# Kernel tuning notes

Hardware: AMD Instinct MI355X
Metric: run time of the kernel (lower is better)

The kernel has to match this reference:

```python
import jax, jax.numpy as jnp
import numpy as np

D_MODEL = 512
N_HEADS = 8
HEAD_DIM = D_MODEL // N_HEADS
B, T = 2, 4096


def setup_inputs() -> dict:
    key = jax.random.key(0)
    k1, k2, k3 = jax.random.split(key, 3)
    scale = 1.0 / np.sqrt(D_MODEL)
    return {
        "x": jax.random.normal(k1, (B, T, D_MODEL), dtype=jnp.float32),
        "w_qkv": jax.random.normal(k2, (D_MODEL, 3 * D_MODEL), dtype=jnp.float32) * scale,
        "b_qkv": jnp.zeros((3 * D_MODEL,), dtype=jnp.float32),
        "w_out": jax.random.normal(k3, (D_MODEL, D_MODEL), dtype=jnp.float32) * scale,
        "b_out": jnp.zeros((D_MODEL,), dtype=jnp.float32),
    }


def reference(x, w_qkv, b_qkv, w_out, b_out):
    Bx, Tx, C = x.shape
    # fused qkv projection -> [B, T, 3, H, Dh] -> split
    qkv = (x @ w_qkv + b_qkv).reshape(Bx, Tx, 3, N_HEADS, HEAD_DIM)
    q = qkv[:, :, 0].transpose(0, 2, 1, 3)  # [B, H, T, Dh]
    k = qkv[:, :, 1].transpose(0, 2, 1, 3)
    v = qkv[:, :, 2].transpose(0, 2, 1, 3)
    # scaled scores with causal mask (materialized [B,H,T,T], as in source)
    att = jnp.einsum("bhqd,bhkd->bhqk", q, k) * (HEAD_DIM ** -0.5)
    causal = jnp.tril(jnp.ones((Tx, Tx), dtype=bool))
    att = jnp.where(causal[None, None], att, -jnp.inf)
    att = jax.nn.softmax(att, axis=-1)
    # dropout = 0.0 (inference-deterministic baseline)
    y = jnp.einsum("bhqk,bhkd->bhqd", att, v)  # [B, H, T, Dh]
    y = y.transpose(0, 2, 1, 3).reshape(Bx, Tx, C)
    return y @ w_out + b_out
```

## Files before the change

### kernel.cpp

```cpp
#include <hip/hip_runtime.h>
#include <cstdint>
#include <cstddef>

typedef __attribute__((ext_vector_type(8)))  __bf16 bf16x8;
typedef __attribute__((ext_vector_type(4)))  float  f32x4;
typedef __attribute__((ext_vector_type(16))) float  f32x16;

#define MFMA16(a, b, c) __builtin_amdgcn_mfma_f32_16x16x32_bf16((a), (b), (c), 0, 0, 0)
#define MFMA32(a, b, c) __builtin_amdgcn_mfma_f32_32x32x16_bf16((a), (b), (c), 0, 0, 0)

#define T_SEQ 4096
#define NHEADS 8
#define DH 64
#define NROWS (2 * NHEADS * T_SEQ)
#define NSPLIT 4
#define NEG_INF (-__builtin_huge_valf())
#define SCALE_Q 0.18033688011112042f

__device__ __forceinline__ unsigned short f2bf(float f) {
  unsigned int u = __float_as_uint(f);
  u += 0x7fffu + ((u >> 16) & 1u);
  return (unsigned short)(u >> 16);
}

__device__ __forceinline__ unsigned int cvtpk(float lo, float hi) {
  unsigned int r;
  asm("v_cvt_pk_bf16_f32 %0, %1, %2" : "=v"(r) : "v"(lo), "v"(hi));
  return r;
}

__device__ __forceinline__ void swap32(unsigned int& x, unsigned int& y) {
  asm("v_permlane32_swap_b32 %0, %1" : "+v"(x), "+v"(y));
}

__device__ __forceinline__ unsigned int pack_bf2(float a, float b) {
  unsigned int au = __float_as_uint(a) + 0x8000u;
  unsigned int bu = __float_as_uint(b) + 0x8000u;
  return (au >> 16) | (bu & 0xffff0000u);
}

__device__ __forceinline__ void gload16(const unsigned short* g, unsigned short* l) {
  __builtin_amdgcn_global_load_lds(
      (const __attribute__((address_space(1))) unsigned short*)g,
      (__attribute__((address_space(3))) unsigned short*)l, 16, 0, 0);
}

__global__ void cvt_x_kernel(const float* __restrict__ x,
                             unsigned short* __restrict__ xb, int n4) {
  int i = blockIdx.x * blockDim.x + threadIdx.x;
  if (i >= n4) return;
  float4 v = ((const float4*)x)[i];
  ushort4 o;
  o.x = f2bf(v.x); o.y = f2bf(v.y); o.z = f2bf(v.z); o.w = f2bf(v.w);
  ((ushort4*)xb)[i] = o;
}

__global__ void cvt_T_kernel(const float* __restrict__ w,
                             unsigned short* __restrict__ wT, int N, int total) {
  int i = blockIdx.x * blockDim.x + threadIdx.x;
  if (i >= total) return;
  int n = i >> 9, k = i & 511;
  wT[i] = f2bf(w[(size_t)k * N + n]);
}

template <int EPI>
__global__ __launch_bounds__(256) void gemm_bt(
    const unsigned short* __restrict__ A,
    const unsigned short* __restrict__ BT,
    const float* __restrict__ bias,
    float* __restrict__ outf,
    unsigned short* __restrict__ oq,
    unsigned short* __restrict__ ok,
    unsigned short* __restrict__ ovT,
    int K) {
  __shared__ alignas(16) unsigned short As[128 * 32];
  __shared__ alignas(16) unsigned short Bs[128 * 32];

  const int t = threadIdx.x;
  const int lane = t & 63;
  const int w = t >> 6;
  const int wr = (w >> 1) * 64;
  const int wc = (w & 1) * 64;
  const int g = lane >> 4, c = lane & 15;
  const int row0 = blockIdx.y * 128, col0 = blockIdx.x * 128;

  const int crow = t >> 2;
  const int ccol = (t & 3) * 8;
  const unsigned short* Ag0 = A + (size_t)(row0 + crow) * K + ccol;
  const unsigned short* Ag1 = A + (size_t)(row0 + 64 + crow) * K + ccol;
  const unsigned short* Bg0 = BT + (size_t)(col0 + crow) * K + ccol;
  const unsigned short* Bg1 = BT + (size_t)(col0 + 64 + crow) * K + ccol;

  f32x4 acc[4][4] = {};

  for (int k0 = 0; k0 < K; k0 += 32) {
    int4 a0 = *(const int4*)(Ag0 + k0);
    int4 a1 = *(const int4*)(Ag1 + k0);
    int4 b0 = *(const int4*)(Bg0 + k0);
    int4 b1 = *(const int4*)(Bg1 + k0);
    __syncthreads();
    *(int4*)&As[crow * 32 + ccol] = a0;
    *(int4*)&As[(64 + crow) * 32 + ccol] = a1;
    *(int4*)&Bs[crow * 32 + ccol] = b0;
    *(int4*)&Bs[(64 + crow) * 32 + ccol] = b1;
    __syncthreads();

    bf16x8 af[4], bfr[4];
#pragma unroll
    for (int m = 0; m < 4; ++m)
      af[m] = *(const bf16x8*)&As[(wr + m * 16 + c) * 32 + g * 8];
#pragma unroll
    for (int n = 0; n < 4; ++n)
      bfr[n] = *(const bf16x8*)&Bs[(wc + n * 16 + c) * 32 + g * 8];
#pragma unroll
    for (int m = 0; m < 4; ++m)
#pragma unroll
      for (int n = 0; n < 4; ++n)
        acc[m][n] = MFMA16(af[m], bfr[n], acc[m][n]);
  }

#pragma unroll
  for (int m = 0; m < 4; ++m) {
#pragma unroll
    for (int n = 0; n < 4; ++n) {
      const int col = col0 + wc + n * 16 + c;
      const float bv = bias[col];
      if constexpr (EPI == 0) {
        const int which = col >> 9;
        const int h = (col >> 6) & 7;
        const int dh = col & 63;
        const int r0 = row0 + wr + m * 16 + g * 4;
        const int bb = r0 >> 12;
        const int tt0 = r0 & 4095;
        if (which == 2) {
          ushort4 pk;
          pk.x = f2bf(acc[m][n][0] + bv);
          pk.y = f2bf(acc[m][n][1] + bv);
          pk.z = f2bf(acc[m][n][2] + bv);
          pk.w = f2bf(acc[m][n][3] + bv);
          *(ushort4*)&ovT[((size_t)((bb * NHEADS + h) * DH + dh)) * T_SEQ + tt0] = pk;
        } else {
          unsigned short* dst = (which == 0) ? oq : ok;
          const float sc = (which == 0) ? SCALE_Q : 1.0f;
#pragma unroll
          for (int i = 0; i < 4; ++i) {
            const size_t idx =
                ((size_t)((bb * NHEADS + h) * T_SEQ + tt0 + i)) * DH + dh;
            dst[idx] = f2bf((acc[m][n][i] + bv) * sc);
          }
        }
      } else {
#pragma unroll
        for (int i = 0; i < 4; ++i) {
          const int row = row0 + wr + m * 16 + g * 4 + i;
          outf[(size_t)row * 512 + col] = acc[m][n][i] + bv;
        }
      }
    }
  }
}

__global__ __launch_bounds__(256, 4) void attn_kernel(
    const unsigned short* __restrict__ qb,
    const unsigned short* __restrict__ kb,
    const unsigned short* __restrict__ vtb,
    unsigned short* __restrict__ opart,
    float* __restrict__ sb) {
  const int bh = blockIdx.x;
  const int y = blockIdx.y;
  const int hv = blockIdx.z;
  const int w = threadIdx.x >> 6;
  const int lane = threadIdx.x & 63;
  const int q32 = lane & 31;
  const int h = lane >> 5;
  const int swb = (lane & 7) << 4;

  __shared__ alignas(16) unsigned short Ks[2][64 * 64];
  __shared__ alignas(16) unsigned short Vs[2][64 * 64];

  const unsigned short* Qp  = qb + (size_t)bh * T_SEQ * DH;
  const unsigned short* Kp  = kb + (size_t)bh * T_SEQ * DH;
  const unsigned short* VTp = vtb + (size_t)bh * DH * T_SEQ;

  unsigned short* obh = opart + (size_t)hv * NROWS * DH;
  float* sbh = sb + (size_t)hv * NROWS + (size_t)bh * T_SEQ;

  const int l8 = lane >> 3, lc = lane & 7;
  const int swzE = 8 * (lc ^ l8);
  const unsigned short* Ksrc0 = Kp + (size_t)(16 * w + l8) * DH + swzE;
  const unsigned short* Ksrc1 = Kp + (size_t)(16 * w + 8 + l8) * DH + swzE;
  const unsigned short* Vsrc0 = VTp + (size_t)(16 * w + l8) * T_SEQ + swzE;
  const unsigned short* Vsrc1 = VTp + (size_t)(16 * w + 8 + l8) * T_SEQ + swzE;

#define STAGE(B, J0) do {                                              \
    gload16(Ksrc0 + (size_t)(J0) * DH, &Ks[B][(2 * w) * 512]);         \
    gload16(Ksrc1 + (size_t)(J0) * DH, &Ks[B][(2 * w + 1) * 512]);     \
    gload16(Vsrc0 + (J0), &Vs[B][(2 * w) * 512]);                      \
    gload16(Vsrc1 + (J0), &Vs[B][(2 * w + 1) * 512]);                  \
  } while (0)

  for (int pass = 0; pass < 2; ++pass) {
    const int sbk = pass ? (31 - y) : y;
    const int qw = sbk * 128 + w * 32;
    const int ntp = 2 * sbk + 2;
    const int t0 = (ntp * hv) >> 2;
    const int t1 = (ntp * (hv + 1)) >> 2;
    const int tlast = (qw + 31) >> 6;

    bf16x8 qf[4];
#pragma unroll
    for (int d = 0; d < 4; ++d)
      qf[d] = *(const bf16x8*)&Qp[(size_t)(qw + q32) * DH + 16 * d + 8 * h];

    f32x16 acc0 = {}, acc1 = {};
    float mi = NEG_INF;
    float li = 0.f;

    STAGE(0, t0 * 64);
    __syncthreads();
    int cur = 0;

    for (int t = t0; t < t1; ++t) {
      if (t + 1 < t1) STAGE(cur ^ 1, (t + 1) * 64);

      if (t <= tlast) {
        const char* Kb = (const char*)&Ks[cur][0];
        const char* Vb = (const char*)&Vs[cur][0];

        f32x16 s0 = {}, s1 = {};
#pragma unroll
        for (int d = 0; d < 4; ++d) {
          bf16x8 kf0 = *(const bf16x8*)(Kb + q32 * 128 +
                                        ((32 * d + 16 * h) ^ swb));
          bf16x8 kf1 = *(const bf16x8*)(Kb + (32 + q32) * 128 +
                                        ((32 * d + 16 * h) ^ swb));
          s0 = MFMA32(kf0, qf[d], s0);
          s1 = MFMA32(kf1, qf[d], s1);
        }

        if (t == tlast) {
          const int qq = qw + q32;
          const int kb0 = t * 64 + 4 * h;
#pragma unroll
          for (int r = 0; r < 16; ++r) {
            const int ko = kb0 + (r & 3) + 8 * (r >> 2);
            if (ko > qq) s0[r] = NEG_INF;
            if (ko + 32 > qq) s1[r] = NEG_INF;
          }
        }

        float mv[8];
#pragma unroll
        for (int i = 0; i < 8; ++i)
          mv[i] = fmaxf(fmaxf(s0[2 * i], s0[2 * i + 1]),
                        fmaxf(s1[2 * i], s1[2 * i + 1]));
        float mloc = fmaxf(fmaxf(fmaxf(mv[0], mv[1]), fmaxf(mv[2], mv[3])),
                           fmaxf(fmaxf(mv[4], mv[5]), fmaxf(mv[6], mv[7])));
        mloc = fmaxf(mloc, __shfl_xor(mloc, 32));

        if (__ballot(mloc > mi + 8.0f) != 0ull) {
          const float mn = fmaxf(mi, mloc);
          const float scq = exp2f(mi - mn);
          mi = mn;
          li *= scq;
#pragma unroll
          for (int r = 0; r < 16; ++r) { acc0[r] *= scq; acc1[r] *= scq; }
        }

        float ls = 0.f;
#pragma unroll
        for (int kk = 0; kk < 4; ++kk) {
          float pv[8];
#pragma unroll
          for (int e = 0; e < 8; ++e) {
            const float sv = (kk < 2) ? s0[(kk & 1) * 8 + e]
                                      : s1[(kk & 1) * 8 + e];
            pv[e] = exp2f(sv - mi);
          }
          ls += ((pv[0] + pv[1]) + (pv[2] + pv[3])) +
                ((pv[4] + pv[5]) + (pv[6] + pv[7]));
          unsigned int a0 = cvtpk(pv[0], pv[1]);
          unsigned int a1 = cvtpk(pv[2], pv[3]);
          unsigned int b0 = cvtpk(pv[4], pv[5]);
          unsigned int b1 = cvtpk(pv[6], pv[7]);
          swap32(a0, b0);
          swap32(a1, b1);
          union { unsigned int u[4]; bf16x8 v; } pf;
          pf.u[0] = a0; pf.u[1] = a1; pf.u[2] = b0; pf.u[3] = b1;

          bf16x8 vf0 = *(const bf16x8*)(Vb + q32 * 128 +
                                        ((32 * kk + 16 * h) ^ swb));
          bf16x8 vf1 = *(const bf16x8*)(Vb + (32 + q32) * 128 +
                                        ((32 * kk + 16 * h) ^ swb));
          acc0 = MFMA32(vf0, pf.v, acc0);
          acc1 = MFMA32(vf1, pf.v, acc1);
        }
        ls += __shfl_xor(ls, 32);
        li += ls;
      }

      __syncthreads();
      cur ^= 1;
    }

    if (lane < 32) sbh[qw + lane] = (li > 0.f) ? (mi + log2f(li)) : NEG_INF;
    const float inv = (li > 0.f) ? 1.0f / li : 0.f;
    const size_t base = ((size_t)bh * T_SEQ + qw + q32) * DH;
#pragma unroll
    for (int dt = 0; dt < 2; ++dt) {
#pragma unroll
      for (int p4 = 0; p4 < 4; ++p4) {
        const float v0 = (dt ? acc1[4 * p4 + 0] : acc0[4 * p4 + 0]) * inv;
        const float v1 = (dt ? acc1[4 * p4 + 1] : acc0[4 * p4 + 1]) * inv;
        const float v2 = (dt ? acc1[4 * p4 + 2] : acc0[4 * p4 + 2]) * inv;
        const float v3 = (dt ? acc1[4 * p4 + 3] : acc0[4 * p4 + 3]) * inv;
        const int d0 = 32 * dt + 8 * p4 + 4 * h;
        *(unsigned int*)&obh[base + d0]     = cvtpk(v0, v1);
        *(unsigned int*)&obh[base + d0 + 2] = cvtpk(v2, v3);
      }
    }
  }
#undef STAGE
}

__global__ __launch_bounds__(256) void merge_kernel(
    const unsigned short* __restrict__ opart,
    const float* __restrict__ sb,
    unsigned short* __restrict__ yb) {
  const int t = threadIdx.x;
  const int r = blockIdx.x * 32 + (t >> 3);
  const int dseg = (t & 7) * 8;
  float s[NSPLIT];
#pragma unroll
  for (int i = 0; i < NSPLIT; ++i) s[i] = sb[(size_t)i * NROWS + r];
  const float S = fmaxf(fmaxf(s[0], s[1]), fmaxf(s[2], s[3]));
  float a[NSPLIT], wsum = 0.f;
#pragma unroll
  for (int i = 0; i < NSPLIT; ++i) { a[i] = exp2f(s[i] - S); wsum += a[i]; }
  const float inv = 1.0f / wsum;
  float acc[8] = {};
#pragma unroll
  for (int i = 0; i < NSPLIT; ++i) {
    const float ai = a[i] * inv;
    const uint4 u = *(const uint4*)&opart[(size_t)i * NROWS * DH +
                                          (size_t)r * DH + dseg];
    const unsigned int* pu = (const unsigned int*)&u;
#pragma unroll
    for (int j = 0; j < 4; ++j) {
      acc[2 * j]     += ai * __uint_as_float(pu[j] << 16);
      acc[2 * j + 1] += ai * __uint_as_float(pu[j] & 0xffff0000u);
    }
  }
  unsigned int ow[4];
#pragma unroll
  for (int j = 0; j < 4; ++j) ow[j] = pack_bf2(acc[2 * j], acc[2 * j + 1]);
  const int bh = r >> 12, q = r & 4095;
  const int bb = bh >> 3, hh = bh & 7;
  *(uint4*)&yb[((size_t)(bb * T_SEQ + q)) * 512 + hh * DH + dseg] = *(uint4*)ow;
}

extern "C" void kernel_launch(void* const* d_in, const int* in_sizes, int n_in,
                              void* d_out, int out_size, void* d_ws, size_t ws_size,
                              hipStream_t stream) {
  const float* x     = (const float*)d_in[0];
  const float* w_qkv = (const float*)d_in[1];
  const float* b_qkv = (const float*)d_in[2];
  const float* w_out = (const float*)d_in[3];
  const float* b_out = (const float*)d_in[4];
  float* out = (float*)d_out;

  char* p = (char*)d_ws;
  unsigned short* xb    = (unsigned short*)p; p += (size_t)8192 * 512 * 2;
  unsigned short* wqkvT = (unsigned short*)p; p += (size_t)1536 * 512 * 2;
  unsigned short* woutT = (unsigned short*)p; p += (size_t)512 * 512 * 2;
  unsigned short* qbuf  = (unsigned short*)p; p += (size_t)16 * T_SEQ * DH * 2;
  unsigned short* kbuf  = (unsigned short*)p; p += (size_t)16 * T_SEQ * DH * 2;
  unsigned short* vtbuf = (unsigned short*)p; p += (size_t)16 * T_SEQ * DH * 2;
  unsigned short* ybuf  = (unsigned short*)p; p += (size_t)8192 * 512 * 2;
  unsigned short* opart = (unsigned short*)p; p += (size_t)NSPLIT * NROWS * DH * 2;
  float*          sbuf  = (float*)p;          p += (size_t)NSPLIT * NROWS * 4;

  cvt_x_kernel<<<4096, 256, 0, stream>>>(x, xb, 8192 * 512 / 4);
  cvt_T_kernel<<<3072, 256, 0, stream>>>(w_qkv, wqkvT, 1536, 1536 * 512);
  cvt_T_kernel<<<1024, 256, 0, stream>>>(w_out, woutT, 512, 512 * 512);

  gemm_bt<0><<<dim3(12, 64), 256, 0, stream>>>(xb, wqkvT, b_qkv, nullptr,
                                               qbuf, kbuf, vtbuf, 512);
  attn_kernel<<<dim3(16, 16, NSPLIT), 256, 0, stream>>>(qbuf, kbuf, vtbuf,
                                                        opart, sbuf);
  merge_kernel<<<NROWS / 32, 256, 0, stream>>>(opart, sbuf, ybuf);
  gemm_bt<1><<<dim3(4, 64), 256, 0, stream>>>(ybuf, woutT, b_out, out,
                                              nullptr, nullptr, nullptr, 512);
}
```

Measured before the change: 138.1 us.

## Double-buffer GEMM LDS tiles with direct global-to-LDS prefetch

```diff
diff --git a/kernel.cpp b/kernel.cpp
--- a/kernel.cpp
+++ b/kernel.cpp
@@ -73,8 +73,8 @@
     unsigned short* __restrict__ ok,
     unsigned short* __restrict__ ovT,
     int K) {
-  __shared__ alignas(16) unsigned short As[128 * 32];
-  __shared__ alignas(16) unsigned short Bs[128 * 32];
+  __shared__ alignas(16) unsigned short As[2][128 * 32];
+  __shared__ alignas(16) unsigned short Bs[2][128 * 32];
 
   const int t = threadIdx.x;
   const int lane = t & 63;
@@ -84,40 +84,46 @@
   const int g = lane >> 4, c = lane & 15;
   const int row0 = blockIdx.y * 128, col0 = blockIdx.x * 128;
 
-  const int crow = t >> 2;
-  const int ccol = (t & 3) * 8;
-  const unsigned short* Ag0 = A + (size_t)(row0 + crow) * K + ccol;
-  const unsigned short* Ag1 = A + (size_t)(row0 + 64 + crow) * K + ccol;
-  const unsigned short* Bg0 = BT + (size_t)(col0 + crow) * K + ccol;
-  const unsigned short* Bg1 = BT + (size_t)(col0 + 64 + crow) * K + ccol;
+  const int sr = t >> 2;
+  const int sc = (t & 3) * 8;
+  const unsigned short* Asrc0 = A + (size_t)(row0 + sr) * K + sc;
+  const unsigned short* Asrc1 = A + (size_t)(row0 + 64 + sr) * K + sc;
+  const unsigned short* Bsrc0 = BT + (size_t)(col0 + sr) * K + sc;
+  const unsigned short* Bsrc1 = BT + (size_t)(col0 + 64 + sr) * K + sc;
+
+#define STAGE_G(B, K0) do {                                    \
+    gload16(Asrc0 + (K0), &As[B][w * 512]);                    \
+    gload16(Asrc1 + (K0), &As[B][2048 + w * 512]);             \
+    gload16(Bsrc0 + (K0), &Bs[B][w * 512]);                    \
+    gload16(Bsrc1 + (K0), &Bs[B][2048 + w * 512]);             \
+  } while (0)
 
   f32x4 acc[4][4] = {};
 
+  STAGE_G(0, 0);
+  __syncthreads();
+  int cur = 0;
+
   for (int k0 = 0; k0 < K; k0 += 32) {
-    int4 a0 = *(const int4*)(Ag0 + k0);
-    int4 a1 = *(const int4*)(Ag1 + k0);
-    int4 b0 = *(const int4*)(Bg0 + k0);
-    int4 b1 = *(const int4*)(Bg1 + k0);
-    __syncthreads();
-    *(int4*)&As[crow * 32 + ccol] = a0;
-    *(int4*)&As[(64 + crow) * 32 + ccol] = a1;
-    *(int4*)&Bs[crow * 32 + ccol] = b0;
-    *(int4*)&Bs[(64 + crow) * 32 + ccol] = b1;
-    __syncthreads();
+    if (k0 + 32 < K) STAGE_G(cur ^ 1, k0 + 32);
 
     bf16x8 af[4], bfr[4];
 #pragma unroll
     for (int m = 0; m < 4; ++m)
-      af[m] = *(const bf16x8*)&As[(wr + m * 16 + c) * 32 + g * 8];
+      af[m] = *(const bf16x8*)&As[cur][(wr + m * 16 + c) * 32 + g * 8];
 #pragma unroll
     for (int n = 0; n < 4; ++n)
-      bfr[n] = *(const bf16x8*)&Bs[(wc + n * 16 + c) * 32 + g * 8];
+      bfr[n] = *(const bf16x8*)&Bs[cur][(wc + n * 16 + c) * 32 + g * 8];
 #pragma unroll
     for (int m = 0; m < 4; ++m)
 #pragma unroll
       for (int n = 0; n < 4; ++n)
         acc[m][n] = MFMA16(af[m], bfr[n], acc[m][n]);
+
+    __syncthreads();
+    cur ^= 1;
   }
+#undef STAGE_G
 
 #pragma unroll
   for (int m = 0; m < 4; ++m) {
@@ -141,12 +147,12 @@
           *(ushort4*)&ovT[((size_t)((bb * NHEADS + h) * DH + dh)) * T_SEQ + tt0] = pk;
         } else {
           unsigned short* dst = (which == 0) ? oq : ok;
-          const float sc = (which == 0) ? SCALE_Q : 1.0f;
+          const float sc2 = (which == 0) ? SCALE_Q : 1.0f;
 #pragma unroll
           for (int i = 0; i < 4; ++i) {
             const size_t idx =
                 ((size_t)((bb * NHEADS + h) * T_SEQ + tt0 + i)) * DH + dh;
-            dst[idx] = f2bf((acc[m][n][i] + bv) * sc);
+            dst[idx] = f2bf((acc[m][n][i] + bv) * sc2);
           }
         }
       } else {
```

After: 133.6 us. 3.2% less time.
